# Kernel tuning notes

Measured on AMD Instinct MI355X. Metric: run time of the kernel, lower is better.

## Reference

```python
import math
import jax, jax.numpy as jnp
import numpy as np

DIM = 128
BITS = 3

def _normal_ppf(p):
    return math.sqrt(2.0) * jax.scipy.special.erfinv(2.0 * p - 1.0)

def _pack_indices(indices, bits):
    vpb = max(1, 8 // bits)
    d = indices.shape[-1]
    padded_d = (d + vpb - 1) // vpb * vpb
    if padded_d > d:
        pad = [(0, 0)] * (indices.ndim - 1) + [(0, padded_d - d)]
        indices = jnp.pad(indices, pad)
    r = indices.astype(jnp.uint8).reshape(*indices.shape[:-1], -1, vpb)
    shifts = (jnp.arange(vpb) * bits).astype(jnp.uint8)
    return jnp.sum(r << shifts, axis=-1, dtype=jnp.uint8)

def _unpack_indices(packed, bits, d):
    vpb = max(1, 8 // bits)
    mask = jnp.uint8((1 << bits) - 1)
    shifts = (jnp.arange(vpb) * bits).astype(jnp.uint8)
    u = ((packed[..., None] >> shifts) & mask).reshape(*packed.shape[:-1], -1)
    return u[..., :d].astype(jnp.int32)

def setup_inputs() -> dict:
    key = jax.random.key(0)
    k1, k2 = jax.random.split(key)
    k = jax.random.normal(k1, (2, 32, 8192, DIM), dtype=jnp.float32)
    # random orthogonal metric scaled so y = E @ k_unit has ~unit-variance coords
    Q = np.linalg.qr(np.asarray(jax.random.normal(k2, (DIM, DIM))))[0].astype(np.float32)
    E = jnp.asarray(Q * math.sqrt(DIM))
    E_inv = jnp.asarray(Q.T / math.sqrt(DIM))
    n_levels = 2 ** BITS
    probs = jnp.linspace(0.0, 1.0, n_levels + 2)[1:-1]
    centroids = _normal_ppf(probs).astype(jnp.float32)
    bp = jnp.linspace(0.0, 1.0, n_levels + 1)
    boundaries = _normal_ppf(jnp.clip(bp, 1e-6, 1.0 - 1e-6))
    decision_boundaries = boundaries[1:-1].astype(jnp.float32)  # interior boundaries only
    return {"k": k, "E": E, "E_inv": E_inv, "centroids": centroids,
            "decision_boundaries": decision_boundaries}

def reference(k, E, E_inv, centroids, decision_boundaries):
    # quantize
    norms = jnp.linalg.norm(k, axis=-1)                       # (..., )
    k_unit = k / (norms[..., None] + 1e-10)
    y = jnp.matmul(k_unit.astype(jnp.float32), E.T)           # (..., dim)
    idx = jnp.searchsorted(decision_boundaries, y)            # torch right=False == side='left'
    packed = _pack_indices(idx, BITS)                          # (..., dim//2) uint8
    # dequantize
    idx2 = _unpack_indices(packed, BITS, DIM)
    y_hat = centroids[idx2]
    k_hat = jnp.matmul(y_hat.astype(jnp.float32), E_inv.T)
    return (k_hat * norms[..., None]).astype(E.dtype)
```

## Files before the change

kernel.cpp:

```cpp
#include <hip/hip_runtime.h>


#define D 128
#define TAU_FIX 1.2e-4f
#define TAU 1.5e-6
#define DFAR 1.35e-7
#define F_HARD 0.175f
#define F_SLOP 0.155f

typedef __attribute__((ext_vector_type(8))) short  bf16x8;
typedef __attribute__((ext_vector_type(8))) unsigned short us8;
typedef __attribute__((ext_vector_type(4))) float  f32x4;

#define SW(row, slot) (((row) << 7) + (((slot) ^ ((row) & 7)) << 3))

__device__ __forceinline__ unsigned short f2bf(float f) {
    unsigned int u = __float_as_uint(f);
    return (unsigned short)((u + 0x7FFFu + ((u >> 16) & 1u)) >> 16);
}
__device__ __forceinline__ float bf2f(unsigned short h) {
    return __uint_as_float(((unsigned int)h) << 16);
}
__device__ __forceinline__ unsigned int cvtpk(float a, float b) {
    unsigned int w;
    asm("v_cvt_pk_bf16_f32 %0, %1, %2" : "=v"(w) : "v"(a), "v"(b));
    return w;
}

__global__ void smaq_prep(const float* __restrict__ Eg,
                          unsigned short* __restrict__ ws16,
                          float* __restrict__ rmaxg)
{
    const int t = blockIdx.x * 256 + threadIdx.x;
    for (int idx = t; idx < D * D; idx += 2048) {
        const int i = idx >> 7, j = idx & (D - 1);
        const float e = Eg[idx];
        const unsigned short eh = f2bf(e);
        const unsigned short el = f2bf(e - bf2f(eh));
        ws16[idx]               = eh;
        ws16[16384 + idx]       = el;
        ws16[32768 + j * D + i] = eh;
        ws16[49152 + j * D + i] = el;
    }
    if (t < D) {
        const float4* er = reinterpret_cast<const float4*>(Eg + (size_t)t * D);
        float mx = 0.f;
        #pragma unroll 8
        for (int j = 0; j < 32; ++j) {
            const float4 e4 = er[j];
            mx = fmaxf(mx, fmaxf(fmaxf(fabsf(e4.x), fabsf(e4.y)),
                                 fmaxf(fabsf(e4.z), fabsf(e4.w))));
        }
        rmaxg[t] = mx;
    }
}

__device__ __noinline__ double fixup_dot(const float4* __restrict__ kr,
                                         const float4* __restrict__ er,
                                         double inv) {
    double a0 = 0, a1 = 0, a2 = 0, a3 = 0;
    #pragma unroll 8
    for (int j = 0; j < 32; ++j) {
        const float4 k4 = kr[j], e4 = er[j];
        a0 = fma((double)e4.x, (double)k4.x, a0);
        a1 = fma((double)e4.y, (double)k4.y, a1);
        a2 = fma((double)e4.z, (double)k4.z, a2);
        a3 = fma((double)e4.w, (double)k4.w, a3);
    }
    return ((a0 + a1) + (a2 + a3)) * inv;
}

__global__ __launch_bounds__(512, 4)
void smaq_quant(const float* __restrict__ kglob,
                const float* __restrict__ Eg,
                const float* __restrict__ centg,
                const float* __restrict__ dbg,
                const unsigned short* __restrict__ ws16,
                const float* __restrict__ rmaxg,
                unsigned int* __restrict__ idxg,
                float* __restrict__ scrg)
{
    __shared__ unsigned short Ehs[D * 128];
    __shared__ unsigned short Els[D * 128];
    __shared__ float  gapL[7];
    __shared__ double bnddL[7];

    const int t  = threadIdx.x;
    const int w  = t >> 6;
    const int l  = t & 63;
    const int lr = l & 15;
    const int lq = l >> 4;
    const long rowbase = (long)blockIdx.x * 64;

    const int rt16   = (w & 3) * 16;
    const int ihb    = (w >> 2) * 64;
    const int r_mine = rt16 + lr;

    const float* kp = kglob + (rowbase + r_mine) * D;
    float4 kv[8];
    #pragma unroll
    for (int ks = 0; ks < 4; ++ks) {
        kv[2 * ks]     = *reinterpret_cast<const float4*>(kp + ks * 32 + lq * 8);
        kv[2 * ks + 1] = *reinterpret_cast<const float4*>(kp + ks * 32 + lq * 8 + 4);
    }

    #pragma unroll
    for (int s = 0; s < 8; ++s) {
        const int c = t + s * 512;
        const us8 v = *reinterpret_cast<const us8*>(
            ws16 + (c >> 11) * 16384 + (c & 2047) * 8);
        const int ch = c & 2047;
        unsigned short* dst = (c >> 11) ? Els : Ehs;
        *reinterpret_cast<us8*>(dst + SW(ch >> 4, ch & 15)) = v;
    }
    if (t < 7) {
        bnddL[t] = (double)dbg[t];
        gapL[t]  = centg[t + 1] - centg[t];
    }

    double s2 = 0.0;
    #pragma unroll
    for (int s = 0; s < 8; ++s) {
        const float4 v = kv[s];
        s2 = fma((double)v.x, (double)v.x, s2);
        s2 = fma((double)v.y, (double)v.y, s2);
        s2 = fma((double)v.z, (double)v.z, s2);
        s2 = fma((double)v.w, (double)v.w, s2);
    }
    s2 += __shfl_xor(s2, 16, 64);
    s2 += __shfl_xor(s2, 32, 64);
    const double nd   = sqrt(s2);
    const double invr = 1.0 / (nd + 1e-10);
    const float  invf = (float)invr;
    const float  scr  = (float)(nd * (1.0 / 128.0));
    if (((w >> 2) == 0) && lq == 0) scrg[rowbase + r_mine] = scr;
    __syncthreads();

    f32x4 acc[4];
    #pragma unroll
    for (int it = 0; it < 4; ++it) acc[it] = (f32x4){0.f, 0.f, 0.f, 0.f};

    #pragma unroll
    for (int ks = 0; ks < 4; ++ks) {
        const float4 a = kv[2 * ks], b = kv[2 * ks + 1];
        const float kf[8] = {a.x * invf, a.y * invf, a.z * invf, a.w * invf,
                             b.x * invf, b.y * invf, b.z * invf, b.w * invf};
        uint4 hw, lw;
        unsigned int* hp = &hw.x;
        unsigned int* lp = &lw.x;
        #pragma unroll
        for (int j = 0; j < 4; ++j) {
            const float f0 = kf[2 * j], f1 = kf[2 * j + 1];
            const unsigned int h = cvtpk(f0, f1);
            const float r0 = f0 - __uint_as_float(h << 16);
            const float r1 = f1 - __uint_as_float(h & 0xFFFF0000u);
            hp[j] = h;
            lp[j] = cvtpk(r0, r1);
        }
        const bf16x8 Bh = *reinterpret_cast<const bf16x8*>(&hw);
        const bf16x8 Bl = *reinterpret_cast<const bf16x8*>(&lw);
        #pragma unroll
        for (int it = 0; it < 4; ++it) {
            const int aoff = SW(ihb + it * 16 + lr, 4 * ks + lq);
            const bf16x8 Ah = *reinterpret_cast<const bf16x8*>(Ehs + aoff);
            const bf16x8 Al = *reinterpret_cast<const bf16x8*>(Els + aoff);
            acc[it] = __builtin_amdgcn_mfma_f32_16x16x32_bf16(Ah, Bh, acc[it], 0, 0, 0);
            acc[it] = __builtin_amdgcn_mfma_f32_16x16x32_bf16(Ah, Bl, acc[it], 0, 0, 0);
            acc[it] = __builtin_amdgcn_mfma_f32_16x16x32_bf16(Al, Bh, acc[it], 0, 0, 0);
            acc[it] = __builtin_amdgcn_mfma_f32_16x16x32_bf16(Al, Bl, acc[it], 0, 0, 0);
        }
    }

    float bnd[7];
    #pragma unroll
    for (int m = 0; m < 7; ++m) bnd[m] = dbg[m];

    #pragma unroll
    for (int it = 0; it < 4; ++it) {
        unsigned int pack = 0;
        #pragma unroll
        for (int reg = 0; reg < 4; ++reg) {
            const int i = ihb + it * 16 + lq * 4 + reg;
            const float y = acc[it][reg];
            int code = 0;
            float dmin = fabsf(y - bnd[0]);
            #pragma unroll
            for (int m = 0; m < 7; ++m) {
                if (m) dmin = fminf(dmin, fabsf(y - bnd[m]));
                code += (bnd[m] < y) ? 1 : 0;
            }
            if (dmin < TAU_FIX) {
                const double yd = fixup_dot(
                    reinterpret_cast<const float4*>(kp),
                    reinterpret_cast<const float4*>(Eg + (size_t)i * D), invr);
                double dm = 1e300;
                int idx2 = 0, ms = 0;
                #pragma unroll
                for (int m = 0; m < 7; ++m) {
                    const double d = fabs(yd - bnddL[m]);
                    if (d < dm) { dm = d; ms = m; }
                    idx2 += (bnddL[m] < yd) ? 1 : 0;
                }
                code = idx2;
                if (dm < TAU) {
                    const float F = gapL[ms] * rmaxg[i] * scr;
                    if (F > F_HARD) {
                    } else if (F > F_SLOP) {
                        if (dm <= DFAR) code = 8 + ms;
                    } else {
                        code = 8 + ms;
                    }
                }
            }
            pack |= (unsigned int)code << (8 * reg);
        }
        idxg[((rowbase + r_mine) * D + ihb + it * 16 + lq * 4) >> 2] = pack;
    }
}

__global__ __launch_bounds__(512, 4)
void smaq_dequant(const unsigned char* __restrict__ idxg,
                  const float* __restrict__ scrg,
                  const float* __restrict__ centg,
                  const float* __restrict__ dbg,
                  const unsigned short* __restrict__ ws16,
                  float* __restrict__ out)
{
    __shared__ unsigned short Ehs[D * 128];
    __shared__ unsigned short Els[D * 128];
    __shared__ unsigned int lutpk[15];

    const int t  = threadIdx.x;
    const int w  = t >> 6;
    const int l  = t & 63;
    const int lr = l & 15;
    const int lq = l >> 4;
    const long rowbase = (long)blockIdx.x * 64;

    const int rt16   = (w & 3) * 16;
    const int jhb    = (w >> 2) * 64;
    const int r_mine = rt16 + lr;

    #pragma unroll
    for (int s = 0; s < 8; ++s) {
        const int c = t + s * 512;
        const us8 v = *reinterpret_cast<const us8*>(
            ws16 + 32768 + (c >> 11) * 16384 + (c & 2047) * 8);
        const int ch = c & 2047;
        unsigned short* dst = (c >> 11) ? Els : Ehs;
        *reinterpret_cast<us8*>(dst + SW(ch >> 4, ch & 15)) = v;
    }
    if (t < 15) {
        float v;
        if (t < 8) v = centg[t];
        else       v = 0.5f * (centg[t - 8] + centg[t - 7]);
        const unsigned short hh = f2bf(v);
        const unsigned short ll = f2bf(v - bf2f(hh));
        lutpk[t] = ((unsigned int)hh << 16) | ll;
    }

    const float scrr = scrg[rowbase + r_mine];
    const unsigned char* ir = idxg + (rowbase + r_mine) * D;
    __syncthreads();

    bf16x8 Yh[4], Yl[4];
    #pragma unroll
    for (int ks = 0; ks < 4; ++ks) {
        const uint2 b8 = *reinterpret_cast<const uint2*>(ir + ks * 32 + lq * 8);
        #pragma unroll
        for (int e = 0; e < 4; ++e) {
            const unsigned int pk = lutpk[(b8.x >> (8 * e)) & 255u];
            Yh[ks][e] = (short)(pk >> 16);
            Yl[ks][e] = (short)(pk & 0xFFFF);
        }
        #pragma unroll
        for (int e = 0; e < 4; ++e) {
            const unsigned int pk = lutpk[(b8.y >> (8 * e)) & 255u];
            Yh[ks][4 + e] = (short)(pk >> 16);
            Yl[ks][4 + e] = (short)(pk & 0xFFFF);
        }
    }

    #pragma unroll
    for (int jt = 0; jt < 4; ++jt) {
        const int jrow = jhb + jt * 16 + lr;
        f32x4 a2 = (f32x4){0.f, 0.f, 0.f, 0.f};
        #pragma unroll
        for (int ks = 0; ks < 4; ++ks) {
            const int aoff = SW(jrow, 4 * ks + lq);
            const bf16x8 At  = *reinterpret_cast<const bf16x8*>(Ehs + aoff);
            const bf16x8 Atl = *reinterpret_cast<const bf16x8*>(Els + aoff);
            a2 = __builtin_amdgcn_mfma_f32_16x16x32_bf16(At,  Yh[ks], a2, 0, 0, 0);
            a2 = __builtin_amdgcn_mfma_f32_16x16x32_bf16(At,  Yl[ks], a2, 0, 0, 0);
            a2 = __builtin_amdgcn_mfma_f32_16x16x32_bf16(Atl, Yh[ks], a2, 0, 0, 0);
        }
        const int j0 = jhb + jt * 16 + lq * 4;
        float4 o;
        o.x = a2[0] * scrr; o.y = a2[1] * scrr;
        o.z = a2[2] * scrr; o.w = a2[3] * scrr;
        *reinterpret_cast<float4*>(out + (rowbase + r_mine) * D + j0) = o;
    }
}

__global__ __launch_bounds__(1024, 4)
__attribute__((amdgpu_waves_per_eu(4, 4)))
void smaq_fused(const float* __restrict__ kglob,
                const float* __restrict__ Eg,
                const float* __restrict__ centg,
                const float* __restrict__ dbg,
                const unsigned short* __restrict__ ws16,
                const float* __restrict__ rmaxg,
                float* __restrict__ out,
                int nrows)
{
    __shared__ unsigned short Ehs[D * 128];
    __shared__ unsigned short Els[D * 128];
    __shared__ unsigned short Yq2[2 * 128 * 128];
    __shared__ float  centL[8], gapL[7], midL[7];
    __shared__ double bnddL[7];

    unsigned short* const Yqh = Yq2;
    unsigned short* const Yql = Yq2 + 128 * 128;
    float* const Kst = reinterpret_cast<float*>(Yq2);

#define KSW(row, slot) (((row) << 7) + (((slot) ^ (((row) & 7) << 2)) << 2))
    const int t  = threadIdx.x;
    const int w  = t >> 6;
    const int l  = t & 63;
    const int lr = l & 15;
    const int lq = l >> 4;
    const long rowbase = (long)blockIdx.x * 128;
    const int rt16   = (w & 7) * 16;
    const int ihb    = (w >> 3) * 64;
    const int r_mine = rt16 + lr;

    #pragma unroll
    for (int s = 0; s < 4; ++s) {
        const int c = t + s * 1024;
        const us8 v = *reinterpret_cast<const us8*>(
            ws16 + (c >> 11) * 16384 + (c & 2047) * 8);
        const int ch = c & 2047;
        unsigned short* dst = (c >> 11) ? Els : Ehs;
        *reinterpret_cast<us8*>(dst + SW(ch >> 4, ch & 15)) = v;
    }
    if (t < 8) {
        const float c = centg[t];
        centL[t] = c;
        if (t < 7) {
            bnddL[t] = (double)dbg[t];
            gapL[t]  = centg[t + 1] - c;
            midL[t]  = 0.5f * (centg[t + 1] + c);
        }
    }

    const float* kp = kglob + (rowbase + r_mine) * D;
    double s2 = 0.0;
    #pragma unroll
    for (int ks = 0; ks < 4; ++ks) {
        const float4 a = *reinterpret_cast<const float4*>(kp + ks * 32 + lq * 8);
        const float4 b = *reinterpret_cast<const float4*>(kp + ks * 32 + lq * 8 + 4);
        s2 = fma((double)a.x, (double)a.x, s2);
        s2 = fma((double)a.y, (double)a.y, s2);
        s2 = fma((double)a.z, (double)a.z, s2);
        s2 = fma((double)a.w, (double)a.w, s2);
        s2 = fma((double)b.x, (double)b.x, s2);
        s2 = fma((double)b.y, (double)b.y, s2);
        s2 = fma((double)b.z, (double)b.z, s2);
        s2 = fma((double)b.w, (double)b.w, s2);
        const int s0 = ks * 8 + lq * 2;
        *reinterpret_cast<float4*>(Kst + KSW(r_mine, s0))     = a;
        *reinterpret_cast<float4*>(Kst + KSW(r_mine, s0 + 1)) = b;
    }
    s2 += __shfl_xor(s2, 16, 64);
    s2 += __shfl_xor(s2, 32, 64);
    const double nd   = sqrt(s2);
    const double invr = 1.0 / (nd + 1e-10);
    const float  scr  = (float)(nd * (1.0 / 128.0));
    asm volatile("" ::: "memory");

    bf16x8 Bh[4], Bl[4];
    #pragma unroll
    for (int ks = 0; ks < 4; ++ks) {
        const int s0 = ks * 8 + lq * 2;
        const float4 a = *reinterpret_cast<const float4*>(Kst + KSW(r_mine, s0));
        const float4 b = *reinterpret_cast<const float4*>(Kst + KSW(r_mine, s0 + 1));
        const float vv[8] = {a.x, a.y, a.z, a.w, b.x, b.y, b.z, b.w};
        #pragma unroll
        for (int e = 0; e < 8; ++e) {
            const float kf = (float)((double)vv[e] * invr);
            const unsigned short hh = f2bf(kf);
            const unsigned short hl = f2bf(kf - bf2f(hh));
            Bh[ks][e] = (short)hh;
            Bl[ks][e] = (short)hl;
        }
    }
    __syncthreads();

    f32x4 acc[4];
    #pragma unroll
    for (int it = 0; it < 4; ++it) acc[it] = (f32x4){0.f, 0.f, 0.f, 0.f};
    #pragma unroll
    for (int it = 0; it < 4; ++it) {
        const int arow = ihb + it * 16 + lr;
        #pragma unroll
        for (int ks = 0; ks < 4; ++ks) {
            const int aoff = SW(arow, 4 * ks + lq);
            const bf16x8 Ah = *reinterpret_cast<const bf16x8*>(Ehs + aoff);
            const bf16x8 Al = *reinterpret_cast<const bf16x8*>(Els + aoff);
            acc[it] = __builtin_amdgcn_mfma_f32_16x16x32_bf16(Ah, Bh[ks], acc[it], 0, 0, 0);
            acc[it] = __builtin_amdgcn_mfma_f32_16x16x32_bf16(Ah, Bl[ks], acc[it], 0, 0, 0);
            acc[it] = __builtin_amdgcn_mfma_f32_16x16x32_bf16(Al, Bh[ks], acc[it], 0, 0, 0);
            acc[it] = __builtin_amdgcn_mfma_f32_16x16x32_bf16(Al, Bl[ks], acc[it], 0, 0, 0);
        }
    }
    __syncthreads();

    us8 etreg[4];
    #pragma unroll
    for (int s = 0; s < 4; ++s) {
        const int c = t + s * 1024;
        etreg[s] = *reinterpret_cast<const us8*>(
            ws16 + 32768 + (c >> 11) * 16384 + (c & 2047) * 8);
    }

    float bnd[7];
    unsigned int centpk[8];
    #pragma unroll
    for (int m = 0; m < 7; ++m) bnd[m] = dbg[m];
    #pragma unroll
    for (int m = 0; m < 8; ++m) {
        const float c = centg[m];
        const unsigned short hh = f2bf(c);
        const unsigned short ll = f2bf(c - bf2f(hh));
        centpk[m] = ((unsigned int)hh << 16) | ll;
    }

    #pragma unroll
    for (int it = 0; it < 4; ++it) {
        unsigned int pk4[4];
        #pragma unroll
        for (int reg = 0; reg < 4; ++reg) {
            const int i = ihb + it * 16 + lq * 4 + reg;
            const float y = acc[it][reg];
            unsigned int pk = centpk[0];
            float dmin = fabsf(y - bnd[0]);
            #pragma unroll
            for (int m = 0; m < 7; ++m) {
                if (m) dmin = fminf(dmin, fabsf(y - bnd[m]));
                pk = (bnd[m] < y) ? centpk[m + 1] : pk;
            }
            if (dmin < TAU_FIX) {
                const double yd = fixup_dot(
                    reinterpret_cast<const float4*>(kglob + (rowbase + r_mine) * D),
                    reinterpret_cast<const float4*>(Eg + (size_t)i * D), invr);
                double dm = 1e300;
                float yq2 = centL[0], gsel = gapL[0], msel = midL[0];
                #pragma unroll
                for (int m = 0; m < 7; ++m) {
                    const double d = fabs(yd - bnddL[m]);
                    const bool lt = d < dm;
                    dm   = lt ? d : dm;
                    gsel = lt ? gapL[m] : gsel;
                    msel = lt ? midL[m] : msel;
                    yq2  = (bnddL[m] < yd) ? centL[m + 1] : yq2;
                }
                float yh = yq2;
                if (dm < TAU) {
                    const float F = gsel * rmaxg[i] * scr;
                    if (F > F_HARD) {
                    } else if (F > F_SLOP) {
                        if (dm <= DFAR) yh = msel;
                    } else {
                        yh = msel;
                    }
                }
                const unsigned short hh = f2bf(yh);
                const unsigned short ll = f2bf(yh - bf2f(hh));
                pk = ((unsigned int)hh << 16) | ll;
            }
            pk4[reg] = pk;
        }
        const int slot = ((ihb + it * 16) >> 3) + (lq >> 1);
        const int off  = SW(r_mine, slot) + (lq & 1) * 4;
        *reinterpret_cast<ushort4*>(Yqh + off) =
            make_ushort4((unsigned short)(pk4[0] >> 16), (unsigned short)(pk4[1] >> 16),
                         (unsigned short)(pk4[2] >> 16), (unsigned short)(pk4[3] >> 16));
        *reinterpret_cast<ushort4*>(Yql + off) =
            make_ushort4((unsigned short)(pk4[0] & 0xFFFF), (unsigned short)(pk4[1] & 0xFFFF),
                         (unsigned short)(pk4[2] & 0xFFFF), (unsigned short)(pk4[3] & 0xFFFF));
    }

    #pragma unroll
    for (int s = 0; s < 4; ++s) {
        const int c = t + s * 1024;
        const int ch = c & 2047;
        unsigned short* dst = (c >> 11) ? Els : Ehs;
        *reinterpret_cast<us8*>(dst + SW(ch >> 4, ch & 15)) = etreg[s];
    }
    __syncthreads();

    bf16x8 Yh[4], Yl[4];
    #pragma unroll
    for (int ks = 0; ks < 4; ++ks) {
        const int off = SW(r_mine, 4 * ks + lq);
        Yh[ks] = *reinterpret_cast<const bf16x8*>(Yqh + off);
        Yl[ks] = *reinterpret_cast<const bf16x8*>(Yql + off);
    }
    #pragma unroll
    for (int jt = 0; jt < 4; ++jt) {
        const int jrow = ihb + jt * 16 + lr;
        f32x4 a2 = (f32x4){0.f, 0.f, 0.f, 0.f};
        #pragma unroll
        for (int ks = 0; ks < 4; ++ks) {
            const int aoff = SW(jrow, 4 * ks + lq);
            const bf16x8 At  = *reinterpret_cast<const bf16x8*>(Ehs + aoff);
            const bf16x8 Atl = *reinterpret_cast<const bf16x8*>(Els + aoff);
            a2 = __builtin_amdgcn_mfma_f32_16x16x32_bf16(At,  Yh[ks], a2, 0, 0, 0);
            a2 = __builtin_amdgcn_mfma_f32_16x16x32_bf16(At,  Yl[ks], a2, 0, 0, 0);
            a2 = __builtin_amdgcn_mfma_f32_16x16x32_bf16(Atl, Yh[ks], a2, 0, 0, 0);
        }
        const int j0 = ihb + jt * 16 + lq * 4;
        float4 o;
        o.x = a2[0] * scr; o.y = a2[1] * scr; o.z = a2[2] * scr; o.w = a2[3] * scr;
        *reinterpret_cast<float4*>(out + (rowbase + r_mine) * D + j0) = o;
    }
#undef KSW
}

extern "C" void kernel_launch(void* const* d_in, const int* in_sizes, int n_in,
                              void* d_out, int out_size, void* d_ws, size_t ws_size,
                              hipStream_t stream)
{
    const float* k    = (const float*)d_in[0];
    const float* E    = (const float*)d_in[1];
    const float* cent = (const float*)d_in[3];
    const float* db   = (const float*)d_in[4];
    float* outp = (float*)d_out;

    unsigned char* wsb = (unsigned char*)d_ws;
    unsigned short* ws16 = (unsigned short*)wsb;
    float* rmaxg = (float*)(wsb + 131072);
    float* scrg  = (float*)(wsb + 131584);
    unsigned char* idxg = wsb + 2228736;
    const size_t need = 2228736ull + 67108864ull;

    const int nrows = in_sizes[0] / D;
    smaq_prep<<<8, 256, 0, stream>>>(E, ws16, rmaxg);
    if (ws_size >= need) {
        smaq_quant<<<nrows / 64, 512, 0, stream>>>(
            k, E, cent, db, ws16, rmaxg, (unsigned int*)idxg, scrg);
        smaq_dequant<<<nrows / 64, 512, 0, stream>>>(
            idxg, scrg, cent, db, ws16, outp);
    } else {
        smaq_fused<<<nrows / 128, 1024, 0, stream>>>(
            k, E, cent, db, ws16, rmaxg, outp, nrows);
    }
}
```

Measured before the change: 378.4 us.

## Split output columns across block pairs to halve LDS per block

Quant and dequant blocks now each handle 128 rows but only half of the 128 output columns, with paired blocks splitting the columns. Each block stages only its 64-row half of the hi/lo bf16 matrices, which halves shared memory per block and raises the launch-bounds occupancy hint from 4 to 8. The cost is that every k row (quant) and index row (dequant) is loaded and normalized by two blocks instead of one, and the norm is computed twice.

```diff
diff --git a/kernel.cpp b/kernel.cpp
--- a/kernel.cpp
+++ b/kernel.cpp
@@ -70,7 +70,7 @@
     return ((a0 + a1) + (a2 + a3)) * inv;
 }
 
-__global__ __launch_bounds__(512, 4)
+__global__ __launch_bounds__(512, 8)
 void smaq_quant(const float* __restrict__ kglob,
                 const float* __restrict__ Eg,
                 const float* __restrict__ centg,
@@ -80,21 +80,20 @@
                 unsigned int* __restrict__ idxg,
                 float* __restrict__ scrg)
 {
-    __shared__ unsigned short Ehs[D * 128];
-    __shared__ unsigned short Els[D * 128];
+    __shared__ unsigned short Ehs[64 * 128];
+    __shared__ unsigned short Els[64 * 128];
     __shared__ float  gapL[7];
     __shared__ double bnddL[7];
 
-    const int t  = threadIdx.x;
-    const int w  = t >> 6;
-    const int l  = t & 63;
-    const int lr = l & 15;
-    const int lq = l >> 4;
-    const long rowbase = (long)blockIdx.x * 64;
-
-    const int rt16   = (w & 3) * 16;
-    const int ihb    = (w >> 2) * 64;
-    const int r_mine = rt16 + lr;
+    const int t    = threadIdx.x;
+    const int w    = t >> 6;
+    const int l    = t & 63;
+    const int lr   = l & 15;
+    const int lq   = l >> 4;
+    const int half = blockIdx.x & 1;
+    const long rowbase = (long)(blockIdx.x >> 1) * 128;
+    const int r_mine = w * 16 + lr;
+    const int ihb    = half * 64;
 
     const float* kp = kglob + (rowbase + r_mine) * D;
     float4 kv[8];
@@ -105,12 +104,12 @@
     }
 
     #pragma unroll
-    for (int s = 0; s < 8; ++s) {
+    for (int s = 0; s < 4; ++s) {
         const int c = t + s * 512;
+        const int plane = c >> 10, ch = c & 1023;
         const us8 v = *reinterpret_cast<const us8*>(
-            ws16 + (c >> 11) * 16384 + (c & 2047) * 8);
-        const int ch = c & 2047;
-        unsigned short* dst = (c >> 11) ? Els : Ehs;
+            ws16 + plane * 16384 + half * 8192 + ch * 8);
+        unsigned short* dst = plane ? Els : Ehs;
         *reinterpret_cast<us8*>(dst + SW(ch >> 4, ch & 15)) = v;
     }
     if (t < 7) {
@@ -133,7 +132,7 @@
     const double invr = 1.0 / (nd + 1e-10);
     const float  invf = (float)invr;
     const float  scr  = (float)(nd * (1.0 / 128.0));
-    if (((w >> 2) == 0) && lq == 0) scrg[rowbase + r_mine] = scr;
+    if (half == 0 && lq == 0) scrg[rowbase + r_mine] = scr;
     __syncthreads();
 
     f32x4 acc[4];
@@ -161,7 +160,7 @@
         const bf16x8 Bl = *reinterpret_cast<const bf16x8*>(&lw);
         #pragma unroll
         for (int it = 0; it < 4; ++it) {
-            const int aoff = SW(ihb + it * 16 + lr, 4 * ks + lq);
+            const int aoff = SW(it * 16 + lr, 4 * ks + lq);
             const bf16x8 Ah = *reinterpret_cast<const bf16x8*>(Ehs + aoff);
             const bf16x8 Al = *reinterpret_cast<const bf16x8*>(Els + aoff);
             acc[it] = __builtin_amdgcn_mfma_f32_16x16x32_bf16(Ah, Bh, acc[it], 0, 0, 0);
@@ -218,7 +217,7 @@
     }
 }
 
-__global__ __launch_bounds__(512, 4)
+__global__ __launch_bounds__(512, 8)
 void smaq_dequant(const unsigned char* __restrict__ idxg,
                   const float* __restrict__ scrg,
                   const float* __restrict__ centg,
@@ -226,28 +225,27 @@
                   const unsigned short* __restrict__ ws16,
                   float* __restrict__ out)
 {
-    __shared__ unsigned short Ehs[D * 128];
-    __shared__ unsigned short Els[D * 128];
+    __shared__ unsigned short Ehs[64 * 128];
+    __shared__ unsigned short Els[64 * 128];
     __shared__ unsigned int lutpk[15];
 
-    const int t  = threadIdx.x;
-    const int w  = t >> 6;
-    const int l  = t & 63;
-    const int lr = l & 15;
-    const int lq = l >> 4;
-    const long rowbase = (long)blockIdx.x * 64;
-
-    const int rt16   = (w & 3) * 16;
-    const int jhb    = (w >> 2) * 64;
-    const int r_mine = rt16 + lr;
-
-    #pragma unroll
-    for (int s = 0; s < 8; ++s) {
+    const int t    = threadIdx.x;
+    const int w    = t >> 6;
+    const int l    = t & 63;
+    const int lr   = l & 15;
+    const int lq   = l >> 4;
+    const int half = blockIdx.x & 1;
+    const long rowbase = (long)(blockIdx.x >> 1) * 128;
+    const int r_mine = w * 16 + lr;
+    const int jhb    = half * 64;
+
+    #pragma unroll
+    for (int s = 0; s < 4; ++s) {
         const int c = t + s * 512;
+        const int plane = c >> 10, ch = c & 1023;
         const us8 v = *reinterpret_cast<const us8*>(
-            ws16 + 32768 + (c >> 11) * 16384 + (c & 2047) * 8);
-        const int ch = c & 2047;
-        unsigned short* dst = (c >> 11) ? Els : Ehs;
+            ws16 + 32768 + plane * 16384 + half * 8192 + ch * 8);
+        unsigned short* dst = plane ? Els : Ehs;
         *reinterpret_cast<us8*>(dst + SW(ch >> 4, ch & 15)) = v;
     }
     if (t < 15) {
@@ -283,11 +281,10 @@
 
     #pragma unroll
     for (int jt = 0; jt < 4; ++jt) {
-        const int jrow = jhb + jt * 16 + lr;
         f32x4 a2 = (f32x4){0.f, 0.f, 0.f, 0.f};
         #pragma unroll
         for (int ks = 0; ks < 4; ++ks) {
-            const int aoff = SW(jrow, 4 * ks + lq);
+            const int aoff = SW(jt * 16 + lr, 4 * ks + lq);
             const bf16x8 At  = *reinterpret_cast<const bf16x8*>(Ehs + aoff);
             const bf16x8 Atl = *reinterpret_cast<const bf16x8*>(Els + aoff);
             a2 = __builtin_amdgcn_mfma_f32_16x16x32_bf16(At,  Yh[ks], a2, 0, 0, 0);
@@ -547,9 +544,10 @@
     const int nrows = in_sizes[0] / D;
     smaq_prep<<<8, 256, 0, stream>>>(E, ws16, rmaxg);
     if (ws_size >= need) {
-        smaq_quant<<<nrows / 64, 512, 0, stream>>>(
+        const int nblk = (nrows / 128) * 2;
+        smaq_quant<<<nblk, 512, 0, stream>>>(
             k, E, cent, db, ws16, rmaxg, (unsigned int*)idxg, scrg);
-        smaq_dequant<<<nrows / 64, 512, 0, stream>>>(
+        smaq_dequant<<<nblk, 512, 0, stream>>>(
             idxg, scrg, cent, db, ws16, outp);
     } else {
         smaq_fused<<<nrows / 128, 1024, 0, stream>>>(
```

Measured after the change: 580.8 us. +53.5%, slower.
